# Kernel tuning notes

Measured on AMD Instinct MI355X. Metric: run time of the kernel, lower is better.

## Reference

```python
import jax, jax.numpy as jnp
import numpy as np

C, K, H = 256, 64, 1024


def squash(t):
    # t: [C, H]; norm = sum of squares over last dim (matches torch code)
    norm = jnp.sum(t * t, axis=-1, keepdims=True)  # [C, 1]
    scale = norm / (1.0 + norm)
    return scale * t / jnp.sqrt(norm)


def setup_inputs() -> dict:
    key = jax.random.key(0)
    k1, k2 = jax.random.split(key)
    encoder_output = jax.random.normal(k1, (C, K, H), dtype=jnp.float32)
    # nn.Linear weight [out, in]; scaled init for numerical sanity
    W = jax.random.normal(k2, (H, H), dtype=jnp.float32) * (1.0 / np.sqrt(H))
    return {"encoder_output": encoder_output, "W": W, "iter_routing": 3}


def reference(encoder_output, W, iter_routing):
    # encoder_output: [C, K, H], W: [H, H] (l_1 weight, no bias)
    # The linear projection is loop-invariant in the original; hoist it.
    x_hat = jnp.einsum('ckh,dh->ckd', encoder_output, W)  # [C, K, H]
    b = jnp.zeros(encoder_output.shape[:2], dtype=encoder_output.dtype)  # [C, K]
    c = None
    for _ in range(iter_routing):
        d = jax.nn.softmax(b, axis=-1)                       # [C, K]
        c_hat = jnp.sum(x_hat * d[..., None], axis=1)        # [C, H]
        c = squash(c_hat)                                    # [C, H]
        b = b + jnp.einsum('ckh,ch->ck', x_hat, c)           # [C, K]
    return c
```

## Files before the change

kernel.cpp:

```cpp
#include <hip/hip_runtime.h>


using f32x4  = __attribute__((ext_vector_type(4))) float;
using f32x2  = __attribute__((ext_vector_type(2))) float;
using bf16x8 = __attribute__((ext_vector_type(8))) __bf16;
using bf16x4 = __attribute__((ext_vector_type(4))) __bf16;

struct BfPair { __bf16 hi, lo; };
__device__ inline BfPair split_bf16(float x) {
    BfPair p;
    p.hi = (__bf16)x;
    p.lo = (__bf16)(x - (float)p.hi);
    return p;
}

template <int MODE>
__device__ __forceinline__ void routing_body(
    const float* __restrict__ enc, const float* __restrict__ y0,
    const float* __restrict__ y1, float* __restrict__ bglob,
    __bf16* __restrict__ s_hi, __bf16* __restrict__ s_lo,
    float (*spart)[1024], float* u_s, float* b_s, float* d_s,
    float* red_s, float* scale_s)
{
    const int t = threadIdx.x, lane = t & 63, w = t >> 6;
    const int c = blockIdx.x;
    const float* E = enc + (size_t)c * 65536;

    float yv = 0.f, sv = 0.f;
    if (MODE > 0) {
        const size_t o = (size_t)c * 1024 + t;
        yv = y0[o] + y1[o];
        sv = (float)s_hi[o] + (float)s_lo[o];
    }

    f32x4 er[4][4];
    #pragma unroll
    for (int r = 0; r < 4; ++r) {
        const float* ek = E + (size_t)(w * 4 + r) * 1024 + lane * 8;
        er[r][0] = *(const f32x4*)(ek);
        er[r][1] = *(const f32x4*)(ek + 4);
        er[r][2] = *(const f32x4*)(ek + 512);
        er[r][3] = *(const f32x4*)(ek + 516);
    }

    if (MODE > 0) {
        u_s[t] = yv;
        float p = yv * sv;
        #pragma unroll
        for (int off = 32; off; off >>= 1) p += __shfl_xor(p, off, 64);
        if (lane == 0) red_s[w] = p;
        __syncthreads();
        if (t == 0) {
            float n = 0.f;
            #pragma unroll
            for (int i = 0; i < 16; ++i) n += red_s[i];
            *scale_s = n / ((1.f + n) * sqrtf(n) + 1e-30f);
        }
        __syncthreads();
        const float scale = *scale_s;
        f32x4 uf[4];
        uf[0] = *(const f32x4*)&u_s[lane * 8];
        uf[1] = *(const f32x4*)&u_s[lane * 8 + 4];
        uf[2] = *(const f32x4*)&u_s[512 + lane * 8];
        uf[3] = *(const f32x4*)&u_s[512 + lane * 8 + 4];
        #pragma unroll
        for (int r = 0; r < 4; ++r) {
            float sum = 0.f;
            #pragma unroll
            for (int q = 0; q < 4; ++q)
                #pragma unroll
                for (int j = 0; j < 4; ++j)
                    sum += er[r][q][j] * uf[q][j];
            #pragma unroll
            for (int off = 32; off; off >>= 1) sum += __shfl_xor(sum, off, 64);
            if (lane == 0) {
                const int k = w * 4 + r;
                const float bv =
                    (MODE == 2 ? bglob[c * 64 + k] : 0.f) + scale * sum;
                bglob[c * 64 + k] = bv;
                b_s[k] = bv;
            }
        }
    }
    __syncthreads();

    if (MODE == 0) {
        if (t < 64) d_s[t] = 1.f / 64.f;
    } else if (t < 64) {
        float bv = b_s[t], m = bv;
        #pragma unroll
        for (int off = 32; off; off >>= 1) m = fmaxf(m, __shfl_xor(m, off, 64));
        const float e = expf(bv - m);
        float sm = e;
        #pragma unroll
        for (int off = 32; off; off >>= 1) sm += __shfl_xor(sm, off, 64);
        d_s[t] = e / sm;
    }
    __syncthreads();

    #pragma unroll
    for (int q = 0; q < 4; ++q) {
        f32x4 p = {};
        #pragma unroll
        for (int r = 0; r < 4; ++r) {
            const float dk = d_s[w * 4 + r];
            #pragma unroll
            for (int j = 0; j < 4; ++j) p[j] += dk * er[r][q][j];
        }
        const int h = (q >> 1) * 512 + lane * 8 + (q & 1) * 4;
        *(f32x4*)&spart[w][h] = p;
    }
    __syncthreads();

    {
        float a = 0.f;
        #pragma unroll
        for (int wv = 0; wv < 16; ++wv) a += spart[wv][t];
        const BfPair p = split_bf16(a);
        s_hi[(size_t)c * 1024 + t] = p.hi;
        s_lo[(size_t)c * 1024 + t] = p.lo;
    }
}

struct QSmem {
    __bf16 a_hi[64 * 64];
    __bf16 a_lo[64 * 64];
    __bf16 b_hi[64 * 64];
    __bf16 b_lo[64 * 64];
};

__device__ __forceinline__ int swz128(int row, int colbyte) {
    return row * 128 + (colbyte ^ ((row & 7) << 4));
}

__device__ __forceinline__ void gemm_q_body(
    const __bf16* __restrict__ Wt_hi, const __bf16* __restrict__ Wt_lo,
    __bf16* __restrict__ Q_hi, __bf16* __restrict__ Q_lo, QSmem* sm, int qb)
{
    const int ti = qb >> 4, tj = qb & 15;
    const int t = threadIdx.x;
    const int lane = t & 63, w = t >> 6;
    const int wr = w >> 2, wc = w & 3;
    const int half = t >> 9;
    const int sr   = (t & 511) >> 3;
    const int scb  = (t & 7) * 16;
    const size_t g = (size_t)((half ? tj : ti) * 64 + sr) * 1024 + scb / 2;
    char* const p_hi = (char*)(half ? sm->b_hi : sm->a_hi) + swz128(sr, scb);
    char* const p_lo = (char*)(half ? sm->b_lo : sm->a_lo) + swz128(sr, scb);

    f32x4 acc = {};
    for (int k0 = 0; k0 < 1024; k0 += 64) {
        if (k0) __syncthreads();
        *(bf16x8*)p_hi = *(const bf16x8*)(Wt_hi + g + k0);
        *(bf16x8*)p_lo = *(const bf16x8*)(Wt_lo + g + k0);
        __syncthreads();
        #pragma unroll
        for (int kk = 0; kk < 2; ++kk) {
            const int cb = kk * 64 + (lane >> 4) * 16;
            const int m = wr * 16 + (lane & 15);
            const int n = wc * 16 + (lane & 15);
            const bf16x8 ah = *(const bf16x8*)((char*)sm->a_hi + swz128(m, cb));
            const bf16x8 al = *(const bf16x8*)((char*)sm->a_lo + swz128(m, cb));
            const bf16x8 bh = *(const bf16x8*)((char*)sm->b_hi + swz128(n, cb));
            const bf16x8 bl = *(const bf16x8*)((char*)sm->b_lo + swz128(n, cb));
            acc = __builtin_amdgcn_mfma_f32_16x16x32_bf16(ah, bh, acc, 0, 0, 0);
            acc = __builtin_amdgcn_mfma_f32_16x16x32_bf16(ah, bl, acc, 0, 0, 0);
            acc = __builtin_amdgcn_mfma_f32_16x16x32_bf16(al, bh, acc, 0, 0, 0);
        }
    }
    const int rr = (lane >> 4) * 4, colb = lane & 15;
    #pragma unroll
    for (int r = 0; r < 4; ++r) {
        const BfPair p = split_bf16(acc[r]);
        const size_t idx =
            (size_t)(ti * 64 + wr * 16 + rr + r) * 1024 +
            tj * 64 + wc * 16 + colb;
        Q_hi[idx] = p.hi;
        Q_lo[idx] = p.lo;
    }
}

template <int MODE, int WITH_Q>
__global__ __launch_bounds__(1024) void routing_q_kernel(
    const float* __restrict__ enc, const float* __restrict__ y0,
    const float* __restrict__ y1, float* __restrict__ bglob,
    __bf16* __restrict__ s_hi, __bf16* __restrict__ s_lo,
    const __bf16* __restrict__ Wt_hi, const __bf16* __restrict__ Wt_lo,
    __bf16* __restrict__ Q_hi, __bf16* __restrict__ Q_lo)
{
    __shared__ union SM {
        struct {
            float spart[16][1024];
            float u_s[1024];
            float b_s[64], d_s[64], red_s[16], scale_s;
        } r;
        QSmem q;
    } sm;

    if (WITH_Q && blockIdx.x >= 256) {
        gemm_q_body(Wt_hi, Wt_lo, Q_hi, Q_lo, &sm.q, blockIdx.x - 256);
        return;
    }
    routing_body<MODE>(enc, y0, y1, bglob, s_hi, s_lo,
                       sm.r.spart, sm.r.u_s, sm.r.b_s, sm.r.d_s,
                       sm.r.red_s, &sm.r.scale_s);
}

template <int CONV>
__global__ __launch_bounds__(256) void gemm_split_kernel(
    const __bf16* __restrict__ Ah, const __bf16* __restrict__ Al,
    const __bf16* __restrict__ Bh, const __bf16* __restrict__ Bl,
    float* __restrict__ C0, float* __restrict__ C1,
    const float* __restrict__ Wsrc, __bf16* __restrict__ Wd_hi,
    __bf16* __restrict__ Wd_lo)
{
    if (CONV && blockIdx.x >= 512) {
        const int b = blockIdx.x - 512;
        const size_t base = (size_t)b * 4096 + (threadIdx.x << 2);
        #pragma unroll
        for (int q = 0; q < 4; ++q) {
            const size_t idx = base + (size_t)q * 1024;
            const f32x4 v = *(const f32x4*)(Wsrc + idx);
            bf16x4 hv, lv;
            #pragma unroll
            for (int j = 0; j < 4; ++j) {
                const BfPair p = split_bf16(v[j]);
                hv[j] = p.hi;
                lv[j] = p.lo;
            }
            *(bf16x4*)(Wd_hi + idx) = hv;
            *(bf16x4*)(Wd_lo + idx) = lv;
        }
        return;
    }

    const int w = threadIdx.x >> 6;
    const int gw = blockIdx.x * 4 + w;
    const int task = gw >> 1;
    const int kh   = gw & 1;
    const int mt   = task >> 6;
    const int nt   = task & 63;
    const int lane = threadIdx.x & 63;
    const int kq   = (lane >> 4) * 8 + kh * 512;
    const size_t aoff = (size_t)(mt * 16 + (lane & 15)) * 1024 + kq;
    const size_t boff = (size_t)(nt * 16 + (lane & 15)) * 1024 + kq;

    f32x4 hh = {}, hl = {}, lh = {};
    #pragma unroll 4
    for (int k0 = 0; k0 < 512; k0 += 32) {
        bf16x8 ah = *(const bf16x8*)(Ah + aoff + k0);
        bf16x8 al = *(const bf16x8*)(Al + aoff + k0);
        bf16x8 bh = *(const bf16x8*)(Bh + boff + k0);
        bf16x8 bl = *(const bf16x8*)(Bl + boff + k0);
        hh = __builtin_amdgcn_mfma_f32_16x16x32_bf16(ah, bh, hh, 0, 0, 0);
        hl = __builtin_amdgcn_mfma_f32_16x16x32_bf16(ah, bl, hl, 0, 0, 0);
        lh = __builtin_amdgcn_mfma_f32_16x16x32_bf16(al, bh, lh, 0, 0, 0);
    }
    f32x4 acc = hh + hl + lh;
    float* Cc = kh ? C1 : C0;
    const int rr = (lane >> 4) * 4, colb = lane & 15;
    #pragma unroll
    for (int r = 0; r < 4; ++r)
        Cc[(size_t)(mt * 16 + rr + r) * 1024 + nt * 16 + colb] = acc[r];
}

__global__ __launch_bounds__(256) void squash_out_kernel(
    const float* __restrict__ chat0, const float* __restrict__ chat1,
    float* __restrict__ outp)
{
    __shared__ float wsum[4];
    const int c = blockIdx.x, t = threadIdx.x;
    const int lane = t & 63, w = t >> 6;
    const size_t o = (size_t)c * 1024 + t * 4;
    f32x4 v = *(const f32x4*)(chat0 + o) + *(const f32x4*)(chat1 + o);
    float ss = v[0]*v[0] + v[1]*v[1] + v[2]*v[2] + v[3]*v[3];
    #pragma unroll
    for (int off = 32; off; off >>= 1) ss += __shfl_xor(ss, off, 64);
    if (lane == 0) wsum[w] = ss;
    __syncthreads();
    const float norm = wsum[0] + wsum[1] + wsum[2] + wsum[3];
    const float scale = norm / ((1.f + norm) * sqrtf(norm) + 1e-30f);
    *(f32x4*)(outp + o) = v * scale;
}

__global__ __launch_bounds__(256) void convert_wt_kernel(
    const float* __restrict__ W, __bf16* __restrict__ Wt_hi,
    __bf16* __restrict__ Wt_lo)
{
    __shared__ float tile[64][65];
    const int bx = blockIdx.x, by = blockIdx.y;
    const int tx = threadIdx.x & 63, ty = threadIdx.x >> 6;
    for (int i = ty; i < 64; i += 4)
        tile[i][tx] = W[(size_t)(by * 64 + i) * 1024 + bx * 64 + tx];
    __syncthreads();
    for (int i = ty; i < 64; i += 4) {
        const size_t idx = (size_t)(bx * 64 + i) * 1024 + by * 64 + tx;
        const BfPair p = split_bf16(tile[tx][i]);
        Wt_hi[idx] = p.hi;
        Wt_lo[idx] = p.lo;
    }
}

__global__ __launch_bounds__(512) void fallback_kernel(
    const float* __restrict__ enc, const float* __restrict__ W,
    float* __restrict__ outp)
{
    __shared__ float u_s[1024], s_s[1024], c_s[1024], chat_s[1024];
    __shared__ float b_s[64], d_s[64], red_s[8];
    const int t = threadIdx.x, lane = t & 63, w = t >> 6;
    const float* erow = enc + (size_t)blockIdx.x * 65536;

    if (t < 64) b_s[t] = 0.f;
    __syncthreads();

    for (int it = 0; it < 3; ++it) {
        if (it > 0) {
            f32x4 uf[4];
            #pragma unroll
            for (int q = 0; q < 2; ++q) {
                uf[2*q]   = *(const f32x4*)&u_s[q*512 + lane*8];
                uf[2*q+1] = *(const f32x4*)&u_s[q*512 + lane*8 + 4];
            }
            for (int r = 0; r < 8; ++r) {
                const int k = w * 8 + r;
                const float* ek = erow + (size_t)k * 1024;
                float sum = 0.f;
                #pragma unroll
                for (int q = 0; q < 2; ++q) {
                    f32x4 e0 = *(const f32x4*)(ek + q*512 + lane*8);
                    f32x4 e1 = *(const f32x4*)(ek + q*512 + lane*8 + 4);
                    #pragma unroll
                    for (int j = 0; j < 4; ++j) {
                        sum += e0[j] * uf[2*q][j];
                        sum += e1[j] * uf[2*q+1][j];
                    }
                }
                #pragma unroll
                for (int off = 32; off; off >>= 1) sum += __shfl_xor(sum, off, 64);
                if (lane == 0) b_s[k] += sum;
            }
            __syncthreads();
        }
        if (t < 64) {
            float bv = b_s[t], m = bv;
            #pragma unroll
            for (int off = 32; off; off >>= 1) m = fmaxf(m, __shfl_xor(m, off, 64));
            float e = expf(bv - m), sm = e;
            #pragma unroll
            for (int off = 32; off; off >>= 1) sm += __shfl_xor(sm, off, 64);
            d_s[t] = e / sm;
        }
        __syncthreads();
        {
            const int h0 = t * 2;
            float a0 = 0.f, a1 = 0.f;
            for (int k = 0; k < 64; ++k) {
                f32x2 ev = *(const f32x2*)(erow + (size_t)k * 1024 + h0);
                a0 += d_s[k] * ev[0]; a1 += d_s[k] * ev[1];
            }
            s_s[h0] = a0; s_s[h0+1] = a1;
        }
        __syncthreads();
        {
            f32x4 sf[4];
            #pragma unroll
            for (int q = 0; q < 2; ++q) {
                sf[2*q]   = *(const f32x4*)&s_s[q*512 + lane*8];
                sf[2*q+1] = *(const f32x4*)&s_s[q*512 + lane*8 + 4];
            }
            for (int r = 0; r < 128; ++r) {
                const int d = w * 128 + r;
                const float* wr = W + (size_t)d * 1024;
                float sum = 0.f;
                #pragma unroll
                for (int q = 0; q < 2; ++q) {
                    f32x4 w0 = *(const f32x4*)(wr + q*512 + lane*8);
                    f32x4 w1 = *(const f32x4*)(wr + q*512 + lane*8 + 4);
                    #pragma unroll
                    for (int j = 0; j < 4; ++j) {
                        sum += w0[j] * sf[2*q][j];
                        sum += w1[j] * sf[2*q+1][j];
                    }
                }
                #pragma unroll
                for (int off = 32; off; off >>= 1) sum += __shfl_xor(sum, off, 64);
                if (lane == 0) chat_s[d] = sum;
            }
        }
        __syncthreads();
        {
            const int h0 = t * 2;
            float v0 = chat_s[h0], v1 = chat_s[h0+1];
            float ss = v0*v0 + v1*v1;
            #pragma unroll
            for (int off = 32; off; off >>= 1) ss += __shfl_xor(ss, off, 64);
            if (lane == 0) red_s[w] = ss;
            __syncthreads();
            float norm = 0.f;
            #pragma unroll
            for (int i = 0; i < 8; ++i) norm += red_s[i];
            const float scale = norm / ((1.f + norm) * sqrtf(norm) + 1e-30f);
            c_s[h0] = v0 * scale; c_s[h0+1] = v1 * scale;
        }
        __syncthreads();
        if (it < 2) {
            const int h0 = t * 2;
            float uu0 = 0.f, uu1 = 0.f;
            for (int d = 0; d < 1024; ++d) {
                f32x2 wv = *(const f32x2*)(W + (size_t)d * 1024 + h0);
                uu0 += c_s[d] * wv[0]; uu1 += c_s[d] * wv[1];
            }
            u_s[h0] = uu0; u_s[h0+1] = uu1;
        } else {
            const int h0 = t * 2;
            f32x2 ov; ov[0] = c_s[h0]; ov[1] = c_s[h0+1];
            *(f32x2*)(outp + (size_t)blockIdx.x * 1024 + h0) = ov;
        }
        __syncthreads();
    }
}

extern "C" void kernel_launch(void* const* d_in, const int* in_sizes, int n_in,
                              void* d_out, int out_size, void* d_ws, size_t ws_size,
                              hipStream_t stream)
{
    const float* enc = (const float*)d_in[0];
    const float* W   = (const float*)d_in[1];
    float* outp = (float*)d_out;
    (void)in_sizes; (void)n_in; (void)out_size;

    char* ws = (char*)d_ws;
    float*  b     = (float*) (ws + 0x000000);
    __bf16* s_hi  = (__bf16*)(ws + 0x080000);
    __bf16* s_lo  = (__bf16*)(ws + 0x100000);
    float*  y0    = (float*) (ws + 0x180000);
    float*  y1    = (float*) (ws + 0x280000);
    __bf16* Wx_hi = (__bf16*)(ws + 0x380000);
    __bf16* Wx_lo = (__bf16*)(ws + 0x580000);
    __bf16* Q_hi  = (__bf16*)(ws + 0x780000);
    __bf16* Q_lo  = (__bf16*)(ws + 0x980000);

    if (ws_size < 0xB80000) {
        fallback_kernel<<<256, 512, 0, stream>>>(enc, W, outp);
        return;
    }

    convert_wt_kernel<<<dim3(16, 16), 256, 0, stream>>>(W, Wx_hi, Wx_lo);

    routing_q_kernel<0, 1><<<512, 1024, 0, stream>>>(
        enc, y0, y1, b, s_hi, s_lo, Wx_hi, Wx_lo, Q_hi, Q_lo);

    gemm_split_kernel<1><<<768, 256, 0, stream>>>(
        s_hi, s_lo, Q_hi, Q_lo, y0, y1, W, Wx_hi, Wx_lo);

    routing_q_kernel<1, 0><<<256, 1024, 0, stream>>>(
        enc, y0, y1, b, s_hi, s_lo, Wx_hi, Wx_lo, Q_hi, Q_lo);

    gemm_split_kernel<0><<<512, 256, 0, stream>>>(
        s_hi, s_lo, Q_hi, Q_lo, y0, y1, nullptr, nullptr, nullptr);

    routing_q_kernel<2, 0><<<256, 1024, 0, stream>>>(
        enc, y0, y1, b, s_hi, s_lo, Wx_hi, Wx_lo, Q_hi, Q_lo);

    gemm_split_kernel<0><<<512, 256, 0, stream>>>(
        s_hi, s_lo, Wx_hi, Wx_lo, y0, y1, nullptr, nullptr, nullptr);

    squash_out_kernel<<<256, 256, 0, stream>>>(y0, y1, outp);
}
```

Measured before the change: 219.1 us.

## Fuse all routing stages into one persistent kernel with grid barriers

Replaces the eight-kernel launch sequence with a single 256-block persistent kernel. Stages are separated by a software grid barrier built on an atomic counter and generation word in workspace, which is zeroed by a memset each call. This removes the launch gaps and tail effects between the many small kernels. In exchange, the GEMM stages now use 64x64 tiles on only 128 blocks (fewer, larger tiles than before), and correctness depends on all 256 blocks being co-resident.

```diff
diff --git a/kernel.cpp b/kernel.cpp
--- a/kernel.cpp
+++ b/kernel.cpp
@@ -5,6 +5,8 @@
 using f32x2  = __attribute__((ext_vector_type(2))) float;
 using bf16x8 = __attribute__((ext_vector_type(8))) __bf16;
 using bf16x4 = __attribute__((ext_vector_type(4))) __bf16;
+
+#define NBLK 256u
 
 struct BfPair { __bf16 hi, lo; };
 __device__ inline BfPair split_bf16(float x) {
@@ -14,16 +16,55 @@
     return p;
 }
 
+struct RoutSM {
+    float spart[16][1024];
+    float u_s[1024];
+    float b_s[64], d_s[64], red_s[16], scale_s;
+};
+struct QSmem {
+    __bf16 a_hi[64 * 64];
+    __bf16 a_lo[64 * 64];
+    __bf16 b_hi[64 * 64];
+    __bf16 b_lo[64 * 64];
+};
+union SM {
+    RoutSM r;
+    QSmem q;
+    float tile[64][65];
+};
+
+__device__ __forceinline__ void gbar(unsigned* cnt, unsigned* gen)
+{
+    __syncthreads();
+    if (threadIdx.x == 0) {
+        __threadfence();
+        const unsigned g =
+            __hip_atomic_load(gen, __ATOMIC_RELAXED, __HIP_MEMORY_SCOPE_AGENT);
+        const unsigned a =
+            __hip_atomic_fetch_add(cnt, 1u, __ATOMIC_ACQ_REL,
+                                   __HIP_MEMORY_SCOPE_AGENT);
+        if (a == NBLK - 1u) {
+            __hip_atomic_store(cnt, 0u, __ATOMIC_RELAXED,
+                               __HIP_MEMORY_SCOPE_AGENT);
+            __hip_atomic_fetch_add(gen, 1u, __ATOMIC_RELEASE,
+                                   __HIP_MEMORY_SCOPE_AGENT);
+        } else {
+            while (__hip_atomic_load(gen, __ATOMIC_ACQUIRE,
+                                     __HIP_MEMORY_SCOPE_AGENT) == g)
+                __builtin_amdgcn_s_sleep(8);
+        }
+        __threadfence();
+    }
+    __syncthreads();
+}
+
 template <int MODE>
 __device__ __forceinline__ void routing_body(
-    const float* __restrict__ enc, const float* __restrict__ y0,
+    int c, const float* __restrict__ enc, const float* __restrict__ y0,
     const float* __restrict__ y1, float* __restrict__ bglob,
-    __bf16* __restrict__ s_hi, __bf16* __restrict__ s_lo,
-    float (*spart)[1024], float* u_s, float* b_s, float* d_s,
-    float* red_s, float* scale_s)
+    __bf16* __restrict__ s_hi, __bf16* __restrict__ s_lo, RoutSM* sm)
 {
     const int t = threadIdx.x, lane = t & 63, w = t >> 6;
-    const int c = blockIdx.x;
     const float* E = enc + (size_t)c * 65536;
 
     float yv = 0.f, sv = 0.f;
@@ -42,27 +83,32 @@
         er[r][2] = *(const f32x4*)(ek + 512);
         er[r][3] = *(const f32x4*)(ek + 516);
     }
+    #pragma unroll
+    for (int r = 0; r < 4; ++r)
+        #pragma unroll
+        for (int q = 0; q < 4; ++q)
+            asm volatile("" : "+v"(er[r][q]));
 
     if (MODE > 0) {
-        u_s[t] = yv;
+        sm->u_s[t] = yv;
         float p = yv * sv;
         #pragma unroll
         for (int off = 32; off; off >>= 1) p += __shfl_xor(p, off, 64);
-        if (lane == 0) red_s[w] = p;
+        if (lane == 0) sm->red_s[w] = p;
         __syncthreads();
         if (t == 0) {
             float n = 0.f;
             #pragma unroll
-            for (int i = 0; i < 16; ++i) n += red_s[i];
-            *scale_s = n / ((1.f + n) * sqrtf(n) + 1e-30f);
-        }
-        __syncthreads();
-        const float scale = *scale_s;
+            for (int i = 0; i < 16; ++i) n += sm->red_s[i];
+            sm->scale_s = n / ((1.f + n) * sqrtf(n) + 1e-30f);
+        }
+        __syncthreads();
+        const float scale = sm->scale_s;
         f32x4 uf[4];
-        uf[0] = *(const f32x4*)&u_s[lane * 8];
-        uf[1] = *(const f32x4*)&u_s[lane * 8 + 4];
-        uf[2] = *(const f32x4*)&u_s[512 + lane * 8];
-        uf[3] = *(const f32x4*)&u_s[512 + lane * 8 + 4];
+        uf[0] = *(const f32x4*)&sm->u_s[lane * 8];
+        uf[1] = *(const f32x4*)&sm->u_s[lane * 8 + 4];
+        uf[2] = *(const f32x4*)&sm->u_s[512 + lane * 8];
+        uf[3] = *(const f32x4*)&sm->u_s[512 + lane * 8 + 4];
         #pragma unroll
         for (int r = 0; r < 4; ++r) {
             float sum = 0.f;
@@ -78,23 +124,23 @@
                 const float bv =
                     (MODE == 2 ? bglob[c * 64 + k] : 0.f) + scale * sum;
                 bglob[c * 64 + k] = bv;
-                b_s[k] = bv;
+                sm->b_s[k] = bv;
             }
         }
     }
     __syncthreads();
 
     if (MODE == 0) {
-        if (t < 64) d_s[t] = 1.f / 64.f;
+        if (t < 64) sm->d_s[t] = 1.f / 64.f;
     } else if (t < 64) {
-        float bv = b_s[t], m = bv;
+        float bv = sm->b_s[t], m = bv;
         #pragma unroll
         for (int off = 32; off; off >>= 1) m = fmaxf(m, __shfl_xor(m, off, 64));
         const float e = expf(bv - m);
-        float sm = e;
-        #pragma unroll
-        for (int off = 32; off; off >>= 1) sm += __shfl_xor(sm, off, 64);
-        d_s[t] = e / sm;
+        float smm = e;
+        #pragma unroll
+        for (int off = 32; off; off >>= 1) smm += __shfl_xor(smm, off, 64);
+        sm->d_s[t] = e / smm;
     }
     __syncthreads();
 
@@ -103,56 +149,53 @@
         f32x4 p = {};
         #pragma unroll
         for (int r = 0; r < 4; ++r) {
-            const float dk = d_s[w * 4 + r];
+            const float dk = sm->d_s[w * 4 + r];
             #pragma unroll
             for (int j = 0; j < 4; ++j) p[j] += dk * er[r][q][j];
         }
         const int h = (q >> 1) * 512 + lane * 8 + (q & 1) * 4;
-        *(f32x4*)&spart[w][h] = p;
+        *(f32x4*)&sm->spart[w][h] = p;
     }
     __syncthreads();
 
     {
         float a = 0.f;
         #pragma unroll
-        for (int wv = 0; wv < 16; ++wv) a += spart[wv][t];
+        for (int wv = 0; wv < 16; ++wv) a += sm->spart[wv][t];
         const BfPair p = split_bf16(a);
         s_hi[(size_t)c * 1024 + t] = p.hi;
         s_lo[(size_t)c * 1024 + t] = p.lo;
     }
 }
 
-struct QSmem {
-    __bf16 a_hi[64 * 64];
-    __bf16 a_lo[64 * 64];
-    __bf16 b_hi[64 * 64];
-    __bf16 b_lo[64 * 64];
-};
-
 __device__ __forceinline__ int swz128(int row, int colbyte) {
     return row * 128 + (colbyte ^ ((row & 7) << 4));
 }
 
-__device__ __forceinline__ void gemm_q_body(
-    const __bf16* __restrict__ Wt_hi, const __bf16* __restrict__ Wt_lo,
-    __bf16* __restrict__ Q_hi, __bf16* __restrict__ Q_lo, QSmem* sm, int qb)
-{
-    const int ti = qb >> 4, tj = qb & 15;
-    const int t = threadIdx.x;
-    const int lane = t & 63, w = t >> 6;
+template <int WQ>
+__device__ __forceinline__ void gemm64_16w(
+    const __bf16* __restrict__ Ah, const __bf16* __restrict__ Al,
+    const __bf16* __restrict__ Bh, const __bf16* __restrict__ Bl,
+    int arow0, int brow0, int kbeg, int kend,
+    float* __restrict__ Cc, __bf16* __restrict__ Qh, __bf16* __restrict__ Ql,
+    int crow0, int ccol0, QSmem* sm)
+{
+    const int t = threadIdx.x, lane = t & 63, w = t >> 6;
     const int wr = w >> 2, wc = w & 3;
     const int half = t >> 9;
     const int sr   = (t & 511) >> 3;
     const int scb  = (t & 7) * 16;
-    const size_t g = (size_t)((half ? tj : ti) * 64 + sr) * 1024 + scb / 2;
+    const __bf16* sh = half ? Bh : Ah;
+    const __bf16* sl = half ? Bl : Al;
+    const size_t g = (size_t)((half ? brow0 : arow0) + sr) * 1024 + scb / 2;
     char* const p_hi = (char*)(half ? sm->b_hi : sm->a_hi) + swz128(sr, scb);
     char* const p_lo = (char*)(half ? sm->b_lo : sm->a_lo) + swz128(sr, scb);
 
     f32x4 acc = {};
-    for (int k0 = 0; k0 < 1024; k0 += 64) {
-        if (k0) __syncthreads();
-        *(bf16x8*)p_hi = *(const bf16x8*)(Wt_hi + g + k0);
-        *(bf16x8*)p_lo = *(const bf16x8*)(Wt_lo + g + k0);
+    for (int k0 = kbeg; k0 < kend; k0 += 64) {
+        __syncthreads();
+        *(bf16x8*)p_hi = *(const bf16x8*)(sh + g + k0);
+        *(bf16x8*)p_lo = *(const bf16x8*)(sl + g + k0);
         __syncthreads();
         #pragma unroll
         for (int kk = 0; kk < 2; ++kk) {
@@ -171,133 +214,113 @@
     const int rr = (lane >> 4) * 4, colb = lane & 15;
     #pragma unroll
     for (int r = 0; r < 4; ++r) {
-        const BfPair p = split_bf16(acc[r]);
-        const size_t idx =
-            (size_t)(ti * 64 + wr * 16 + rr + r) * 1024 +
-            tj * 64 + wc * 16 + colb;
-        Q_hi[idx] = p.hi;
-        Q_lo[idx] = p.lo;
-    }
-}
-
-template <int MODE, int WITH_Q>
-__global__ __launch_bounds__(1024) void routing_q_kernel(
-    const float* __restrict__ enc, const float* __restrict__ y0,
-    const float* __restrict__ y1, float* __restrict__ bglob,
+        const size_t idx = (size_t)(crow0 + wr * 16 + rr + r) * 1024 +
+                           ccol0 + wc * 16 + colb;
+        if (WQ) {
+            const BfPair p = split_bf16(acc[r]);
+            Qh[idx] = p.hi;
+            Ql[idx] = p.lo;
+        } else {
+            Cc[idx] = acc[r];
+        }
+    }
+}
+
+__global__ __launch_bounds__(1024, 4) void fused_kernel(
+    const float* __restrict__ enc, const float* __restrict__ W,
+    float* __restrict__ outp, float* __restrict__ bglob,
     __bf16* __restrict__ s_hi, __bf16* __restrict__ s_lo,
-    const __bf16* __restrict__ Wt_hi, const __bf16* __restrict__ Wt_lo,
-    __bf16* __restrict__ Q_hi, __bf16* __restrict__ Q_lo)
-{
-    __shared__ union SM {
-        struct {
-            float spart[16][1024];
-            float u_s[1024];
-            float b_s[64], d_s[64], red_s[16], scale_s;
-        } r;
-        QSmem q;
-    } sm;
-
-    if (WITH_Q && blockIdx.x >= 256) {
-        gemm_q_body(Wt_hi, Wt_lo, Q_hi, Q_lo, &sm.q, blockIdx.x - 256);
-        return;
-    }
-    routing_body<MODE>(enc, y0, y1, bglob, s_hi, s_lo,
-                       sm.r.spart, sm.r.u_s, sm.r.b_s, sm.r.d_s,
-                       sm.r.red_s, &sm.r.scale_s);
-}
-
-template <int CONV>
-__global__ __launch_bounds__(256) void gemm_split_kernel(
-    const __bf16* __restrict__ Ah, const __bf16* __restrict__ Al,
-    const __bf16* __restrict__ Bh, const __bf16* __restrict__ Bl,
-    float* __restrict__ C0, float* __restrict__ C1,
-    const float* __restrict__ Wsrc, __bf16* __restrict__ Wd_hi,
-    __bf16* __restrict__ Wd_lo)
-{
-    if (CONV && blockIdx.x >= 512) {
-        const int b = blockIdx.x - 512;
-        const size_t base = (size_t)b * 4096 + (threadIdx.x << 2);
-        #pragma unroll
-        for (int q = 0; q < 4; ++q) {
-            const size_t idx = base + (size_t)q * 1024;
-            const f32x4 v = *(const f32x4*)(Wsrc + idx);
-            bf16x4 hv, lv;
-            #pragma unroll
-            for (int j = 0; j < 4; ++j) {
-                const BfPair p = split_bf16(v[j]);
-                hv[j] = p.hi;
-                lv[j] = p.lo;
-            }
-            *(bf16x4*)(Wd_hi + idx) = hv;
-            *(bf16x4*)(Wd_lo + idx) = lv;
-        }
-        return;
-    }
-
-    const int w = threadIdx.x >> 6;
-    const int gw = blockIdx.x * 4 + w;
-    const int task = gw >> 1;
-    const int kh   = gw & 1;
-    const int mt   = task >> 6;
-    const int nt   = task & 63;
-    const int lane = threadIdx.x & 63;
-    const int kq   = (lane >> 4) * 8 + kh * 512;
-    const size_t aoff = (size_t)(mt * 16 + (lane & 15)) * 1024 + kq;
-    const size_t boff = (size_t)(nt * 16 + (lane & 15)) * 1024 + kq;
-
-    f32x4 hh = {}, hl = {}, lh = {};
-    #pragma unroll 4
-    for (int k0 = 0; k0 < 512; k0 += 32) {
-        bf16x8 ah = *(const bf16x8*)(Ah + aoff + k0);
-        bf16x8 al = *(const bf16x8*)(Al + aoff + k0);
-        bf16x8 bh = *(const bf16x8*)(Bh + boff + k0);
-        bf16x8 bl = *(const bf16x8*)(Bl + boff + k0);
-        hh = __builtin_amdgcn_mfma_f32_16x16x32_bf16(ah, bh, hh, 0, 0, 0);
-        hl = __builtin_amdgcn_mfma_f32_16x16x32_bf16(ah, bl, hl, 0, 0, 0);
-        lh = __builtin_amdgcn_mfma_f32_16x16x32_bf16(al, bh, lh, 0, 0, 0);
-    }
-    f32x4 acc = hh + hl + lh;
-    float* Cc = kh ? C1 : C0;
-    const int rr = (lane >> 4) * 4, colb = lane & 15;
-    #pragma unroll
-    for (int r = 0; r < 4; ++r)
-        Cc[(size_t)(mt * 16 + rr + r) * 1024 + nt * 16 + colb] = acc[r];
-}
-
-__global__ __launch_bounds__(256) void squash_out_kernel(
-    const float* __restrict__ chat0, const float* __restrict__ chat1,
-    float* __restrict__ outp)
-{
-    __shared__ float wsum[4];
-    const int c = blockIdx.x, t = threadIdx.x;
-    const int lane = t & 63, w = t >> 6;
-    const size_t o = (size_t)c * 1024 + t * 4;
-    f32x4 v = *(const f32x4*)(chat0 + o) + *(const f32x4*)(chat1 + o);
-    float ss = v[0]*v[0] + v[1]*v[1] + v[2]*v[2] + v[3]*v[3];
-    #pragma unroll
-    for (int off = 32; off; off >>= 1) ss += __shfl_xor(ss, off, 64);
-    if (lane == 0) wsum[w] = ss;
-    __syncthreads();
-    const float norm = wsum[0] + wsum[1] + wsum[2] + wsum[3];
-    const float scale = norm / ((1.f + norm) * sqrtf(norm) + 1e-30f);
-    *(f32x4*)(outp + o) = v * scale;
-}
-
-__global__ __launch_bounds__(256) void convert_wt_kernel(
-    const float* __restrict__ W, __bf16* __restrict__ Wt_hi,
-    __bf16* __restrict__ Wt_lo)
-{
-    __shared__ float tile[64][65];
-    const int bx = blockIdx.x, by = blockIdx.y;
-    const int tx = threadIdx.x & 63, ty = threadIdx.x >> 6;
-    for (int i = ty; i < 64; i += 4)
-        tile[i][tx] = W[(size_t)(by * 64 + i) * 1024 + bx * 64 + tx];
-    __syncthreads();
-    for (int i = ty; i < 64; i += 4) {
-        const size_t idx = (size_t)(bx * 64 + i) * 1024 + by * 64 + tx;
-        const BfPair p = split_bf16(tile[tx][i]);
-        Wt_hi[idx] = p.hi;
-        Wt_lo[idx] = p.lo;
+    float* __restrict__ y0, float* __restrict__ y1,
+    __bf16* __restrict__ Wx_hi, __bf16* __restrict__ Wx_lo,
+    __bf16* __restrict__ Q_hi, __bf16* __restrict__ Q_lo,
+    unsigned* __restrict__ bar)
+{
+    __shared__ union SM sm;
+    const int b = blockIdx.x, t = threadIdx.x;
+    unsigned* cnt = bar;
+    unsigned* gen = bar + 32;
+
+    {
+        const int by = b >> 4, bx4 = b & 15;
+        const int tx = t & 63, tg = t >> 6;
+        for (int i = tg; i < 64; i += 16)
+            sm.tile[i][tx] =
+                W[(size_t)(by * 64 + i) * 1024 + bx4 * 64 + tx];
+        __syncthreads();
+        for (int i = tg; i < 64; i += 16) {
+            const size_t idx = (size_t)(bx4 * 64 + i) * 1024 + by * 64 + tx;
+            const BfPair p = split_bf16(sm.tile[tx][i]);
+            Wx_hi[idx] = p.hi;
+            Wx_lo[idx] = p.lo;
+        }
+    }
+    gbar(cnt, gen);
+
+    {
+        const int ti = b >> 4, tj = b & 15;
+        gemm64_16w<1>(Wx_hi, Wx_lo, Wx_hi, Wx_lo, ti * 64, tj * 64, 0, 1024,
+                      nullptr, Q_hi, Q_lo, ti * 64, tj * 64, &sm.q);
+        __syncthreads();
+        routing_body<0>(b, enc, y0, y1, bglob, s_hi, s_lo, &sm.r);
+    }
+    gbar(cnt, gen);
+
+    if (b < 128) {
+        const int kh = b & 1, tk = b >> 1;
+        const int mt = tk >> 4, nt = tk & 15;
+        gemm64_16w<0>(s_hi, s_lo, Q_hi, Q_lo, mt * 64, nt * 64,
+                      kh * 512, kh * 512 + 512, kh ? y1 : y0,
+                      nullptr, nullptr, mt * 64, nt * 64, &sm.q);
+    } else {
+        const int bb = b - 128;
+        #pragma unroll
+        for (int q = 0; q < 8; ++q) {
+            const size_t idx = (size_t)bb * 8192 + (size_t)q * 1024 + t;
+            const BfPair p = split_bf16(W[idx]);
+            Wx_hi[idx] = p.hi;
+            Wx_lo[idx] = p.lo;
+        }
+    }
+    gbar(cnt, gen);
+
+    routing_body<1>(b, enc, y0, y1, bglob, s_hi, s_lo, &sm.r);
+    gbar(cnt, gen);
+
+    if (b < 128) {
+        const int kh = b & 1, tk = b >> 1;
+        const int mt = tk >> 4, nt = tk & 15;
+        gemm64_16w<0>(s_hi, s_lo, Q_hi, Q_lo, mt * 64, nt * 64,
+                      kh * 512, kh * 512 + 512, kh ? y1 : y0,
+                      nullptr, nullptr, mt * 64, nt * 64, &sm.q);
+    }
+    gbar(cnt, gen);
+
+    routing_body<2>(b, enc, y0, y1, bglob, s_hi, s_lo, &sm.r);
+    gbar(cnt, gen);
+
+    if (b < 128) {
+        const int kh = b & 1, tk = b >> 1;
+        const int mt = tk >> 4, nt = tk & 15;
+        gemm64_16w<0>(s_hi, s_lo, Wx_hi, Wx_lo, mt * 64, nt * 64,
+                      kh * 512, kh * 512 + 512, kh ? y1 : y0,
+                      nullptr, nullptr, mt * 64, nt * 64, &sm.q);
+    }
+    gbar(cnt, gen);
+
+    {
+        const int lane = t & 63, w = t >> 6;
+        const size_t o = (size_t)b * 1024 + t;
+        const float v = y0[o] + y1[o];
+        float ss = v * v;
+        #pragma unroll
+        for (int off = 32; off; off >>= 1) ss += __shfl_xor(ss, off, 64);
+        if (lane == 0) sm.r.red_s[w] = ss;
+        __syncthreads();
+        float norm = 0.f;
+        #pragma unroll
+        for (int i = 0; i < 16; ++i) norm += sm.r.red_s[i];
+        const float scale = norm / ((1.f + norm) * sqrtf(norm) + 1e-30f);
+        outp[o] = v * scale;
     }
 }
 
@@ -430,40 +453,25 @@
     (void)in_sizes; (void)n_in; (void)out_size;
 
     char* ws = (char*)d_ws;
-    float*  b     = (float*) (ws + 0x000000);
-    __bf16* s_hi  = (__bf16*)(ws + 0x080000);
-    __bf16* s_lo  = (__bf16*)(ws + 0x100000);
-    float*  y0    = (float*) (ws + 0x180000);
-    float*  y1    = (float*) (ws + 0x280000);
-    __bf16* Wx_hi = (__bf16*)(ws + 0x380000);
-    __bf16* Wx_lo = (__bf16*)(ws + 0x580000);
-    __bf16* Q_hi  = (__bf16*)(ws + 0x780000);
-    __bf16* Q_lo  = (__bf16*)(ws + 0x980000);
-
-    if (ws_size < 0xB80000) {
+    float*    b     = (float*)   (ws + 0x000000);
+    __bf16*   s_hi  = (__bf16*)  (ws + 0x080000);
+    __bf16*   s_lo  = (__bf16*)  (ws + 0x100000);
+    float*    y0    = (float*)   (ws + 0x180000);
+    float*    y1    = (float*)   (ws + 0x280000);
+    __bf16*   Wx_hi = (__bf16*)  (ws + 0x380000);
+    __bf16*   Wx_lo = (__bf16*)  (ws + 0x580000);
+    __bf16*   Q_hi  = (__bf16*)  (ws + 0x780000);
+    __bf16*   Q_lo  = (__bf16*)  (ws + 0x980000);
+    unsigned* bar   = (unsigned*)(ws + 0xB80000);
+
+    if (ws_size < 0xB80100) {
         fallback_kernel<<<256, 512, 0, stream>>>(enc, W, outp);
         return;
     }
 
-    convert_wt_kernel<<<dim3(16, 16), 256, 0, stream>>>(W, Wx_hi, Wx_lo);
-
-    routing_q_kernel<0, 1><<<512, 1024, 0, stream>>>(
-        enc, y0, y1, b, s_hi, s_lo, Wx_hi, Wx_lo, Q_hi, Q_lo);
-
-    gemm_split_kernel<1><<<768, 256, 0, stream>>>(
-        s_hi, s_lo, Q_hi, Q_lo, y0, y1, W, Wx_hi, Wx_lo);
-
-    routing_q_kernel<1, 0><<<256, 1024, 0, stream>>>(
-        enc, y0, y1, b, s_hi, s_lo, Wx_hi, Wx_lo, Q_hi, Q_lo);
-
-    gemm_split_kernel<0><<<512, 256, 0, stream>>>(
-        s_hi, s_lo, Q_hi, Q_lo, y0, y1, nullptr, nullptr, nullptr);
-
-    routing_q_kernel<2, 0><<<256, 1024, 0, stream>>>(
-        enc, y0, y1, b, s_hi, s_lo, Wx_hi, Wx_lo, Q_hi, Q_lo);
-
-    gemm_split_kernel<0><<<512, 256, 0, stream>>>(
-        s_hi, s_lo, Wx_hi, Wx_lo, y0, y1, nullptr, nullptr, nullptr);
-
-    squash_out_kernel<<<256, 256, 0, stream>>>(y0, y1, outp);
-}
+    hipMemsetAsync(bar, 0, 256, stream);
+
+    fused_kernel<<<256, 1024, 0, stream>>>(
+        enc, W, outp, b, s_hi, s_lo, y0, y1,
+        Wx_hi, Wx_lo, Q_hi, Q_lo, bar);
+}
```

After: 450.1 us. +105.4%, slower.
